# Kernel optimization log

Measured on AMD Instinct MI355X. Metric: run time of the kernel, lower is better.

Reference implementation:

```python
import jax, jax.numpy as jnp
import numpy as np

B, L, D, P = 4, 128, 256, 1024
TU, TB = 86400, 3600  # tu = 24*3600, time_bin = 3600
NEG = float(-2**32 + 1)


def setup_inputs() -> dict:
    key = jax.random.key(0)
    ks = jax.random.split(key, 16)
    src = jax.random.normal(ks[0], (B, L, D), jnp.float32)
    batch_seq_lens = jax.random.randint(ks[1], (B,), L // 2, L + 1, dtype=jnp.int32)
    ts = jnp.sort(jax.random.randint(ks[2], (B, L), 0, 864000, dtype=jnp.int32), axis=1)
    lts = ts + jax.random.randint(ks[3], (B, L), 0, 7200, dtype=jnp.int32)
    s = 0.02
    hour_emb = (jax.random.normal(ks[4], (TU // TB + 2, D), jnp.float32) * s).at[0].set(0.0)  # padding_idx=0
    day_emb = (jax.random.normal(ks[5], (8, D), jnp.float32) * s).at[0].set(0.0)              # padding_idx=0
    wq = jax.random.normal(ks[6], (D, D), jnp.float32) * s
    wk = jax.random.normal(ks[7], (D, D), jnp.float32) * s
    wv = jax.random.normal(ks[8], (D, D), jnp.float32) * s
    wf1 = jax.random.normal(ks[9], (D, D), jnp.float32) * s
    wf2 = jax.random.normal(ks[10], (D, D), jnp.float32) * s
    wdec = jax.random.uniform(ks[11], (P, D), jnp.float32, -0.1, 0.1)  # init_weights uniform(-0.1,0.1)
    z = jnp.zeros((D,), jnp.float32)
    return {
        'src': src, 'hour_emb': hour_emb, 'day_emb': day_emb,
        'wq': wq, 'bq': z, 'wk': wk, 'bk': z, 'wv': wv, 'bv': z,
        'g11': jnp.ones((D,), jnp.float32), 'b11': z,
        'wf1': wf1, 'bf1': z, 'wf2': wf2, 'bf2': z,
        'g12': jnp.ones((D,), jnp.float32), 'b12': z,
        'wdec': wdec, 'bdec': jnp.zeros((P,), jnp.float32),
        'batch_seq_lens': batch_seq_lens,
        'batch_input_seqs_ts': ts,
        'batch_label_seqs_ts': lts,
    }


def _ln(x, g, b):
    m = jnp.mean(x, axis=-1, keepdims=True)
    v = jnp.var(x, axis=-1, keepdims=True)
    return (x - m) * jax.lax.rsqrt(v + 1e-5) * g + b


def reference(src, hour_emb, day_emb, wq, bq, wk, bk, wv, bv, g11, b11,
              wf1, bf1, wf2, bf2, g12, b12, wdec, bdec,
              batch_seq_lens, batch_input_seqs_ts, batch_label_seqs_ts):
    ts, lts = batch_input_seqs_ts, batch_label_seqs_ts
    # per-pair time intervals, [B,L,L]
    diff = ts[:, :, None] - ts[:, None, :]
    hour = (diff % TU) // TB + 2
    # faithful to source: 'if i == j' compares batch index to row position
    hour = jnp.where((jnp.arange(B)[:, None] == jnp.arange(L)[None, :])[:, :, None], 1, hour)
    day = jnp.minimum(diff // TU + 1, 7)
    ldiff = lts[:, :, None] - ts[:, None, :]
    lhour = (ldiff % TU) // TB + 2
    lday = jnp.minimum(ldiff // TU + 1, 7)
    tril = jnp.tril(jnp.ones((L, L), bool))
    rows_valid = jnp.arange(L)[None, :] < batch_seq_lens[:, None]  # [B,L]
    valid = tril[None] & rows_valid[:, :, None]
    # index 0 == padding row (zero embedding), matching zeros-init + padding_idx=0
    hour = jnp.where(valid, hour, 0)
    day = jnp.where(valid, day, 0)
    lhour = jnp.where(valid, lhour, 0)
    lday = jnp.where(valid, lday, 0)
    hE = hour_emb[hour]    # [B,L,L,D]
    dE = day_emb[day]
    lhE = hour_emb[lhour]
    ldE = day_emb[lday]

    Q = src @ wq.T + bq
    K = src @ wk.T + bk
    V = src @ wv.T + bv
    aw = (jnp.einsum('bjd,bkd->bjk', Q, K)
          + jnp.einsum('bjkd,bjd->bjk', hE, Q)
          + jnp.einsum('bjkd,bjd->bjk', dE, Q)) / jnp.sqrt(jnp.float32(D))
    mask = (~tril)[None] | (~rows_valid)[:, :, None]
    aw = jnp.where(mask, NEG, aw)
    aw = jax.nn.softmax(aw, axis=-1)
    x = (jnp.einsum('bjk,bkd->bjd', aw, V)
         + jnp.einsum('bjk,bjkd->bjd', aw, hE)
         + jnp.einsum('bjk,bjkd->bjd', aw, dE))
    x = _ln(x + src, g11, b11)
    f = jnp.maximum(x @ wf1.T + bf1, 0.0) @ wf2.T + bf2  # dropout is identity at eval
    f = _ln(x + f, g12, b12)

    # out4[b,j,k,:] = f[b,k,:] + label interval embeddings
    out4 = f[:, None, :, :] + lhE + ldE            # [B,L,L,D]
    dec = out4 @ wdec.T + bdec                     # [B,L,L,P]
    counts = jnp.arange(1, L + 1, dtype=dec.dtype)
    pooled = jnp.einsum('bjkp,jk->bjp', dec, tril.astype(dec.dtype)) / counts[None, :, None]
    return pooled
```

## Files before the change

kernel.cpp:

```cpp
#include <hip/hip_runtime.h>
#include <hip/hip_bf16.h>

#define LL 128
#define DD 256
#define PP 1024
#define TU_C 86400
#define TB_C 3600
#define NEGF -4294967296.0f

#define FMA4(ACC_, SS_, WW_) { (ACC_).x += (SS_)*(WW_).x; (ACC_).y += (SS_)*(WW_).y; (ACC_).z += (SS_)*(WW_).z; (ACC_).w += (SS_)*(WW_).w; }
#define ADD4(ACC_, WW_) { (ACC_).x += (WW_).x; (ACC_).y += (WW_).y; (ACC_).z += (WW_).z; (ACC_).w += (WW_).w; }

__device__ __forceinline__ float wredSum(float v) {
#pragma unroll
  for (int o = 32; o; o >>= 1) v += __shfl_xor(v, o);
  return v;
}
__device__ __forceinline__ float wredMax(float v) {
#pragma unroll
  for (int o = 32; o; o >>= 1) v = fmaxf(v, __shfl_xor(v, o));
  return v;
}

__global__ __launch_bounds__(256) void k_wt(
    const float* __restrict__ wq, const float* __restrict__ wk,
    const float* __restrict__ wv, const float* __restrict__ wf1,
    const float* __restrict__ wf2, const float* __restrict__ wdec,
    float* __restrict__ wt)
{
  __shared__ float s[32][33];
  const int tile = blockIdx.x;
  const float* src; float* dst; int R, m;
  if (tile < 320) {
    const int mi = tile >> 6; m = tile & 63;
    src = (mi == 0) ? wq : (mi == 1) ? wk : (mi == 2) ? wv : (mi == 3) ? wf1 : wf2;
    dst = wt + mi * 65536; R = 256;
  } else {
    m = tile - 320; src = wdec; dst = wt + 327680; R = 1024;
  }
  const int sr = (m >> 3) * 32, sc0 = (m & 7) * 32;
  const int tx = threadIdx.x & 31, ty = threadIdx.x >> 5;
#pragma unroll
  for (int i = 0; i < 4; ++i)
    s[ty + 8 * i][tx] = src[(sr + ty + 8 * i) * 256 + sc0 + tx];
  __syncthreads();
#pragma unroll
  for (int i = 0; i < 4; ++i)
    dst[(sc0 + ty + 8 * i) * R + sr + tx] = s[tx][ty + 8 * i];
}

__global__ __launch_bounds__(256) void k_qkv(
    const float* __restrict__ src, const float* __restrict__ wt,
    const float* __restrict__ bq, const float* __restrict__ bk,
    const float* __restrict__ bv,
    float* __restrict__ Q, float* __restrict__ KT, float* __restrict__ V)
{
  __shared__ float xs[8][DD];
  __shared__ float ps[4][8][DD];
  const int t = threadIdx.x, l = t & 63, w = t >> 6;
  const int r0 = blockIdx.x * 8;
  const int mat = blockIdx.y;
  const float* wm = wt + mat * 65536;
  for (int i = t; i < 8 * DD; i += 256) xs[i >> 8][i & 255] = src[r0 * DD + i];
  __syncthreads();
  const int col = 4 * l;
  float4 acc[8];
#pragma unroll
  for (int r = 0; r < 8; ++r) acc[r] = (float4){0.f, 0.f, 0.f, 0.f};
  const int e0 = 64 * w;
  for (int e = e0; e < e0 + 64; e += 4) {
    float4 xr[8];
#pragma unroll
    for (int r = 0; r < 8; ++r) xr[r] = *(const float4*)&xs[r][e];
#pragma unroll
    for (int c = 0; c < 4; ++c) {
      const float4 w4 = *(const float4*)(wm + (e + c) * DD + col);
#pragma unroll
      for (int r = 0; r < 8; ++r) {
        const float xv = (c == 0) ? xr[r].x : (c == 1) ? xr[r].y : (c == 2) ? xr[r].z : xr[r].w;
        FMA4(acc[r], xv, w4)
      }
    }
  }
#pragma unroll
  for (int r = 0; r < 8; ++r) *(float4*)&ps[w][r][col] = acc[r];
  __syncthreads();
  const float* bi = (mat == 0) ? bq : (mat == 1) ? bk : bv;
#pragma unroll
  for (int g = 0; g < 2; ++g) {
    const int combo = g * 256 + t;
    const int r = combo >> 6, cgp = combo & 63;
    const int c4 = 4 * cgp;
    float4 o = *(const float4*)(bi + c4);
    ADD4(o, (*(const float4*)&ps[0][r][c4]))
    ADD4(o, (*(const float4*)&ps[1][r][c4]))
    ADD4(o, (*(const float4*)&ps[2][r][c4]))
    ADD4(o, (*(const float4*)&ps[3][r][c4]))
    const int rr = r0 + r;
    if (mat == 1) {
      const int bA = rr >> 7, kA = rr & 127;
      KT[bA * 32768 + (c4 + 0) * 128 + kA] = o.x;
      KT[bA * 32768 + (c4 + 1) * 128 + kA] = o.y;
      KT[bA * 32768 + (c4 + 2) * 128 + kA] = o.z;
      KT[bA * 32768 + (c4 + 3) * 128 + kA] = o.w;
    } else {
      float* op = (mat == 0) ? Q : V;
      *(float4*)(op + rr * DD + c4) = o;
    }
  }
}

__global__ __launch_bounds__(512) void k_attn(
    const float* __restrict__ Q, const float* __restrict__ KT,
    const float* __restrict__ Vm, const float* __restrict__ src,
    const float* __restrict__ hour_emb, const float* __restrict__ day_emb,
    const int* __restrict__ seq_lens, const int* __restrict__ ts_g,
    const float* __restrict__ g11, const float* __restrict__ b11,
    const float* __restrict__ wt1, const float* __restrict__ bf1,
    const float* __restrict__ wt2, const float* __restrict__ bf2,
    const float* __restrict__ g12, const float* __restrict__ b12,
    float* __restrict__ F)
{
  const int b = blockIdx.x >> 6;
  const int j0 = (blockIdx.x & 63) * 2;
  const int t = threadIdx.x, w = t >> 6, l = t & 63;
  const int col = 4 * l;
  __shared__ float qs[2][DD];
  __shared__ int   tsl[LL];
  __shared__ float qhd[2][34];
  __shared__ float whd[2][34];
  __shared__ float red[8];
  __shared__ float ss[2][LL];
  __shared__ float xs2[2][DD];
  __shared__ float hs2[2][DD];
  __shared__ float ps[8][2][DD];
  const int row0 = b * LL + j0;
  qs[t >> 8][t & 255] = Q[row0 * DD + t];
  if (t < LL) tsl[t] = ts_g[b * LL + t];
  if (t < 68) whd[t / 34][t % 34] = 0.f;
  __syncthreads();
  float kdot = 0.f;
  int krow = 0, kidx = 0;
  if (w < 4) {
    krow = w >> 1;
    kidx = ((w & 1) << 6) | l;
    const float* ktb = KT + b * 32768;
    float4 kd = {0.f,0.f,0.f,0.f};
#pragma unroll 8
    for (int e = 0; e < DD; e += 4) {
      const float4 q4 = *(const float4*)&qs[krow][e];
      const float* kp = ktb + e * LL + kidx;
      kd.x += q4.x * kp[0];
      kd.y += q4.y * kp[128];
      kd.z += q4.z * kp[256];
      kd.w += q4.w * kp[384];
    }
    kdot = (kd.x + kd.y) + (kd.z + kd.w);
  } else if (w < 6 && l < 34) {
    const int r = w - 4;
    const float* ep = (l < 26) ? (hour_emb + l * DD) : (day_emb + (l - 26) * DD);
    float4 ed = {0.f,0.f,0.f,0.f};
    for (int e = 0; e < DD; e += 4) {
      const float4 q4 = *(const float4*)&qs[r][e];
      const float4 e4 = *(const float4*)(ep + e);
      ed.x += q4.x * e4.x; ed.y += q4.y * e4.y;
      ed.z += q4.z * e4.z; ed.w += q4.w * e4.w;
    }
    qhd[r][l] = (ed.x + ed.y) + (ed.z + ed.w);
  }
  __syncthreads();
  const int len = seq_lens[b];
  float s = NEGF;
  int hidx = 0, didx = 0;
  if (w < 4) {
    const int jrow = j0 + krow;
    if (kidx <= jrow && jrow < len) {
      const int df = tsl[jrow] - tsl[kidx];
      hidx = (jrow == b) ? 1 : ((df % TU_C) / TB_C + 2);
      didx = min(df / TU_C + 1, 7);
      s = (kdot + qhd[krow][hidx] + qhd[krow][26 + didx]) * 0.0625f;
    }
    const float mv = wredMax(s);
    if (l == 0) red[w] = mv;
  }
  __syncthreads();
  float p = 0.f;
  if (w < 4) {
    const float m = fmaxf(red[2 * krow], red[2 * krow + 1]);
    p = expf(s - m);
    const float sv = wredSum(p);
    if (l == 0) red[4 + w] = sv;
  }
  __syncthreads();
  if (w < 4) {
    const float Z = red[4 + 2 * krow] + red[5 + 2 * krow];
    const float aw = p / Z;
    ss[krow][kidx] = aw;
    atomicAdd(&whd[krow][hidx], aw);
    atomicAdd(&whd[krow][26 + didx], aw);
  }
  __syncthreads();
  {
    float4 a0 = {0.f,0.f,0.f,0.f}, a1 = {0.f,0.f,0.f,0.f};
    const float* vb = Vm + b * LL * DD + col;
    const int k0 = 16 * w;
#pragma unroll
    for (int kk = 0; kk < 16; ++kk) {
      const int k = k0 + kk;
      const float4 v4 = *(const float4*)(vb + k * DD);
      FMA4(a0, ss[0][k], v4)
      FMA4(a1, ss[1][k], v4)
    }
    if (w == 0) {
#pragma unroll
      for (int i = 0; i < 26; ++i)
        FMA4(a0, whd[0][i], *(const float4*)(hour_emb + i * DD + col))
    } else if (w == 1) {
#pragma unroll
      for (int i = 0; i < 26; ++i)
        FMA4(a1, whd[1][i], *(const float4*)(hour_emb + i * DD + col))
    } else if (w == 2) {
#pragma unroll
      for (int i = 0; i < 8; ++i)
        FMA4(a0, whd[0][26 + i], *(const float4*)(day_emb + i * DD + col))
      const float4 s4 = *(const float4*)(src + row0 * DD + col);
      ADD4(a0, s4)
    } else if (w == 3) {
#pragma unroll
      for (int i = 0; i < 8; ++i)
        FMA4(a1, whd[1][26 + i], *(const float4*)(day_emb + i * DD + col))
      const float4 s4 = *(const float4*)(src + (row0 + 1) * DD + col);
      ADD4(a1, s4)
    }
    *(float4*)&ps[w][0][col] = a0;
    *(float4*)&ps[w][1][col] = a1;
  }
  __syncthreads();
  if (w < 2) {
    float4 x = *(const float4*)&ps[0][w][col];
#pragma unroll
    for (int i = 1; i < 8; ++i) ADD4(x, (*(const float4*)&ps[i][w][col]))
    const float sm = wredSum(x.x + x.y + x.z + x.w);
    const float sq = wredSum(x.x*x.x + x.y*x.y + x.z*x.z + x.w*x.w);
    const float mean = sm * (1.f / DD);
    const float rstd = rsqrtf(sq * (1.f / DD) - mean * mean + 1e-5f);
    const float4 g4 = *(const float4*)(g11 + col);
    const float4 b4 = *(const float4*)(b11 + col);
    x.x = (x.x - mean) * rstd * g4.x + b4.x;
    x.y = (x.y - mean) * rstd * g4.y + b4.y;
    x.z = (x.z - mean) * rstd * g4.z + b4.z;
    x.w = (x.w - mean) * rstd * g4.w + b4.w;
    *(float4*)&xs2[w][col] = x;
  }
  __syncthreads();
  {
    float4 a0 = {0.f,0.f,0.f,0.f}, a1 = {0.f,0.f,0.f,0.f};
    const int e0 = 32 * w;
#pragma unroll 8
    for (int ee = 0; ee < 32; ++ee) {
      const int e = e0 + ee;
      const float4 w4 = *(const float4*)(wt1 + e * DD + col);
      FMA4(a0, xs2[0][e], w4)
      FMA4(a1, xs2[1][e], w4)
    }
    *(float4*)&ps[w][0][col] = a0;
    *(float4*)&ps[w][1][col] = a1;
  }
  __syncthreads();
  if (w < 2) {
    float4 h = *(const float4*)(bf1 + col);
#pragma unroll
    for (int i = 0; i < 8; ++i) ADD4(h, (*(const float4*)&ps[i][w][col]))
    h.x = fmaxf(h.x, 0.f); h.y = fmaxf(h.y, 0.f);
    h.z = fmaxf(h.z, 0.f); h.w = fmaxf(h.w, 0.f);
    *(float4*)&hs2[w][col] = h;
  }
  __syncthreads();
  {
    float4 a0 = {0.f,0.f,0.f,0.f}, a1 = {0.f,0.f,0.f,0.f};
    const int e0 = 32 * w;
#pragma unroll 8
    for (int ee = 0; ee < 32; ++ee) {
      const int e = e0 + ee;
      const float4 w4 = *(const float4*)(wt2 + e * DD + col);
      FMA4(a0, hs2[0][e], w4)
      FMA4(a1, hs2[1][e], w4)
    }
    *(float4*)&ps[w][0][col] = a0;
    *(float4*)&ps[w][1][col] = a1;
  }
  __syncthreads();
  if (w < 2) {
    float4 o = *(const float4*)(bf2 + col);
#pragma unroll
    for (int i = 0; i < 8; ++i) ADD4(o, (*(const float4*)&ps[i][w][col]))
    const float4 xr = *(const float4*)&xs2[w][col];
    ADD4(o, xr)
    const float sm = wredSum(o.x + o.y + o.z + o.w);
    const float sq = wredSum(o.x*o.x + o.y*o.y + o.z*o.z + o.w*o.w);
    const float mean = sm * (1.f / DD);
    const float rstd = rsqrtf(sq * (1.f / DD) - mean * mean + 1e-5f);
    const float4 g4 = *(const float4*)(g12 + col);
    const float4 b4 = *(const float4*)(b12 + col);
    o.x = (o.x - mean) * rstd * g4.x + b4.x;
    o.y = (o.y - mean) * rstd * g4.y + b4.y;
    o.z = (o.z - mean) * rstd * g4.z + b4.z;
    o.w = (o.w - mean) * rstd * g4.w + b4.w;
    *(float4*)(F + (row0 + w) * DD + col) = o;
  }
}

__global__ __launch_bounds__(256) void k_decf(
    const float* __restrict__ F,
    const float* __restrict__ hour_emb, const float* __restrict__ day_emb,
    const int* __restrict__ seq_lens, const int* __restrict__ ts_g,
    const int* __restrict__ lts_g,
    const float* __restrict__ wtd, const float* __restrict__ bdec,
    float* __restrict__ out)
{
  const int c0 = blockIdx.x * 256;
  const int r0g = blockIdx.y * 8;
  const int b = r0g >> 7, j0 = r0g & 127;
  const int t = threadIdx.x, l = t & 63, w = t >> 6;
  __shared__ float xs[8][DD];
  __shared__ float cnt[8][34];
  __shared__ float ps[4][8][DD];
  for (int i = t; i < 8 * 34; i += 256) (&cnt[0][0])[i] = 0.f;
  __syncthreads();
  const int len = seq_lens[b];
  const int* ts = ts_g + b * LL;
  const int* lts = lts_g + b * LL;
#pragma unroll
  for (int p = 0; p < 4; ++p) {
    const int idx = p * 256 + t;
    const int jj = idx >> 7, k = idx & 127, j = j0 + jj;
    if (k <= j && j < len) {
      const int ld = lts[j] - ts[k];
      atomicAdd(&cnt[jj][(ld % TU_C) / TB_C + 2], 1.f);
      atomicAdd(&cnt[jj][26 + min(ld / TU_C + 1, 7)], 1.f);
    }
  }
  __syncthreads();
  {
    float he[26], de[8];
#pragma unroll
    for (int i = 0; i < 26; ++i) he[i] = hour_emb[i * DD + t];
#pragma unroll
    for (int i = 0; i < 8; ++i)  de[i] = day_emb[i * DD + t];
    const float* fb = F + b * LL * DD + t;
    float A0 = 0.f, A1 = 0.f, A2 = 0.f, A3 = 0.f;
#pragma unroll 4
    for (int k = 0; k < j0; k += 4) {
      A0 += fb[(k + 0) * DD]; A1 += fb[(k + 1) * DD];
      A2 += fb[(k + 2) * DD]; A3 += fb[(k + 3) * DD];
    }
    float gacc = (A0 + A1) + (A2 + A3);
#pragma unroll
    for (int jj = 0; jj < 8; ++jj) {
      gacc += fb[(j0 + jj) * DD];
      float s0 = 0.f, s1 = 0.f;
#pragma unroll
      for (int i = 0; i < 26; i += 2) {
        s0 += cnt[jj][i] * he[i]; s1 += cnt[jj][i + 1] * he[i + 1];
      }
#pragma unroll
      for (int i = 0; i < 8; i += 2) {
        s0 += cnt[jj][26 + i] * de[i]; s1 += cnt[jj][27 + i] * de[i + 1];
      }
      xs[jj][t] = (gacc + s0 + s1) / (float)(j0 + jj + 1);
    }
  }
  __syncthreads();
  const int col = c0 + 4 * l;
  float4 acc[8];
#pragma unroll
  for (int r = 0; r < 8; ++r) acc[r] = (float4){0.f, 0.f, 0.f, 0.f};
  const int e0 = 64 * w;
  for (int e = e0; e < e0 + 64; e += 4) {
    float4 xr[8];
#pragma unroll
    for (int r = 0; r < 8; ++r) xr[r] = *(const float4*)&xs[r][e];
#pragma unroll
    for (int c = 0; c < 4; ++c) {
      const float4 w4 = *(const float4*)(wtd + (e + c) * PP + col);
#pragma unroll
      for (int r = 0; r < 8; ++r) {
        const float xv = (c == 0) ? xr[r].x : (c == 1) ? xr[r].y : (c == 2) ? xr[r].z : xr[r].w;
        FMA4(acc[r], xv, w4)
      }
    }
  }
#pragma unroll
  for (int r = 0; r < 8; ++r) *(float4*)&ps[w][r][4 * l] = acc[r];
  __syncthreads();
#pragma unroll
  for (int g = 0; g < 2; ++g) {
    const int combo = g * 256 + t;
    const int r = combo >> 6, cgp = combo & 63;
    const int c4 = 4 * cgp;
    float4 o = *(const float4*)(bdec + c0 + c4);
    ADD4(o, (*(const float4*)&ps[0][r][c4]))
    ADD4(o, (*(const float4*)&ps[1][r][c4]))
    ADD4(o, (*(const float4*)&ps[2][r][c4]))
    ADD4(o, (*(const float4*)&ps[3][r][c4]))
    *(float4*)(out + (r0g + r) * PP + c0 + c4) = o;
  }
}

extern "C" void kernel_launch(void* const* d_in, const int* in_sizes, int n_in,
                              void* d_out, int out_size, void* d_ws, size_t ws_size,
                              hipStream_t stream)
{
  (void)in_sizes; (void)n_in; (void)out_size; (void)ws_size;
  const float* src      = (const float*)d_in[0];
  const float* hour_emb = (const float*)d_in[1];
  const float* day_emb  = (const float*)d_in[2];
  const float* wq  = (const float*)d_in[3];
  const float* bq  = (const float*)d_in[4];
  const float* wk  = (const float*)d_in[5];
  const float* bk  = (const float*)d_in[6];
  const float* wv  = (const float*)d_in[7];
  const float* bv  = (const float*)d_in[8];
  const float* g11 = (const float*)d_in[9];
  const float* b11 = (const float*)d_in[10];
  const float* wf1 = (const float*)d_in[11];
  const float* bf1 = (const float*)d_in[12];
  const float* wf2 = (const float*)d_in[13];
  const float* bf2 = (const float*)d_in[14];
  const float* g12 = (const float*)d_in[15];
  const float* b12 = (const float*)d_in[16];
  const float* wdec = (const float*)d_in[17];
  const float* bdec = (const float*)d_in[18];
  const int* seq_lens = (const int*)d_in[19];
  const int* ts  = (const int*)d_in[20];
  const int* lts = (const int*)d_in[21];
  float* out = (float*)d_out;
  float* ws = (float*)d_ws;
  float* WT = ws;
  float* Q  = ws + 589824;
  float* KT = ws + 720896;
  float* V  = ws + 851968;
  float* F  = ws + 983040;

  k_wt  <<<576, 256, 0, stream>>>(wq, wk, wv, wf1, wf2, wdec, WT);
  k_qkv <<<dim3(64, 3), 256, 0, stream>>>(src, WT, bq, bk, bv, Q, KT, V);
  k_attn<<<256, 512, 0, stream>>>(Q, KT, V, src, hour_emb, day_emb, seq_lens, ts,
                                  g11, b11, WT + 196608, bf1, WT + 262144, bf2,
                                  g12, b12, F);
  k_decf<<<dim3(4, 64), 256, 0, stream>>>(F, hour_emb, day_emb, seq_lens, ts, lts,
                                          WT + 327680, bdec, out);
}
```

Baseline: 50.36 us.

## Fuse weight transpose and QKV projection into one kernel launch

Merges the weight-transpose kernel and the QKV projection kernel into a single launch. Blocks 0-191 compute Q/K/V by reading the untransposed wq/wk/wv directly, staging 16-column chunks into LDS, while the remaining blocks transpose only wf1, wf2 and wdec for later kernels. This drops one kernel launch and the dependency of QKV on a transposed copy of its own weights. In exchange the QKV GEMM loop synchronises 16 times per block and does strided, poorly coalesced global loads of the weights.

```diff
diff --git a/kernel.cpp b/kernel.cpp
--- a/kernel.cpp
+++ b/kernel.cpp
@@ -22,91 +22,81 @@
   return v;
 }
 
-__global__ __launch_bounds__(256) void k_wt(
+__global__ __launch_bounds__(256) void k_qkv2(
     const float* __restrict__ wq, const float* __restrict__ wk,
     const float* __restrict__ wv, const float* __restrict__ wf1,
     const float* __restrict__ wf2, const float* __restrict__ wdec,
-    float* __restrict__ wt)
-{
-  __shared__ float s[32][33];
-  const int tile = blockIdx.x;
-  const float* src; float* dst; int R, m;
-  if (tile < 320) {
-    const int mi = tile >> 6; m = tile & 63;
-    src = (mi == 0) ? wq : (mi == 1) ? wk : (mi == 2) ? wv : (mi == 3) ? wf1 : wf2;
-    dst = wt + mi * 65536; R = 256;
-  } else {
-    m = tile - 320; src = wdec; dst = wt + 327680; R = 1024;
-  }
-  const int sr = (m >> 3) * 32, sc0 = (m & 7) * 32;
-  const int tx = threadIdx.x & 31, ty = threadIdx.x >> 5;
-#pragma unroll
-  for (int i = 0; i < 4; ++i)
-    s[ty + 8 * i][tx] = src[(sr + ty + 8 * i) * 256 + sc0 + tx];
-  __syncthreads();
-#pragma unroll
-  for (int i = 0; i < 4; ++i)
-    dst[(sc0 + ty + 8 * i) * R + sr + tx] = s[tx][ty + 8 * i];
-}
-
-__global__ __launch_bounds__(256) void k_qkv(
-    const float* __restrict__ src, const float* __restrict__ wt,
+    const float* __restrict__ src,
     const float* __restrict__ bq, const float* __restrict__ bk,
     const float* __restrict__ bv,
+    float* __restrict__ WT,
     float* __restrict__ Q, float* __restrict__ KT, float* __restrict__ V)
 {
+  const int bx = blockIdx.x;
+  const int t = threadIdx.x;
+  if (bx >= 192) {
+    __shared__ float s[32][33];
+    const int tile = bx - 192;
+    const float* sw; float* dst; int R, m;
+    if (tile < 64)       { sw = wf1;  dst = WT + 196608; R = 256;  m = tile; }
+    else if (tile < 128) { sw = wf2;  dst = WT + 262144; R = 256;  m = tile - 64; }
+    else                 { sw = wdec; dst = WT + 327680; R = 1024; m = tile - 128; }
+    const int sr = (m >> 3) * 32, sc0 = (m & 7) * 32;
+    const int tx = t & 31, ty = t >> 5;
+#pragma unroll
+    for (int i = 0; i < 4; ++i)
+      s[ty + 8 * i][tx] = sw[(sr + ty + 8 * i) * 256 + sc0 + tx];
+    __syncthreads();
+#pragma unroll
+    for (int i = 0; i < 4; ++i)
+      dst[(sc0 + ty + 8 * i) * R + sr + tx] = s[tx][ty + 8 * i];
+    return;
+  }
+  const int mat = bx >> 6;
+  const int r0 = (bx & 63) * 8;
+  const float* wm = (mat == 0) ? wq : (mat == 1) ? wk : wv;
   __shared__ float xs[8][DD];
-  __shared__ float ps[4][8][DD];
-  const int t = threadIdx.x, l = t & 63, w = t >> 6;
-  const int r0 = blockIdx.x * 8;
-  const int mat = blockIdx.y;
-  const float* wm = wt + mat * 65536;
+  __shared__ float wlds[16][260];
   for (int i = t; i < 8 * DD; i += 256) xs[i >> 8][i & 255] = src[r0 * DD + i];
-  __syncthreads();
-  const int col = 4 * l;
-  float4 acc[8];
-#pragma unroll
-  for (int r = 0; r < 8; ++r) acc[r] = (float4){0.f, 0.f, 0.f, 0.f};
-  const int e0 = 64 * w;
-  for (int e = e0; e < e0 + 64; e += 4) {
-    float4 xr[8];
-#pragma unroll
-    for (int r = 0; r < 8; ++r) xr[r] = *(const float4*)&xs[r][e];
-#pragma unroll
-    for (int c = 0; c < 4; ++c) {
-      const float4 w4 = *(const float4*)(wm + (e + c) * DD + col);
-#pragma unroll
-      for (int r = 0; r < 8; ++r) {
-        const float xv = (c == 0) ? xr[r].x : (c == 1) ? xr[r].y : (c == 2) ? xr[r].z : xr[r].w;
-        FMA4(acc[r], xv, w4)
-      }
-    }
-  }
-#pragma unroll
-  for (int r = 0; r < 8; ++r) *(float4*)&ps[w][r][col] = acc[r];
-  __syncthreads();
+  const int cg = t & 63, w = t >> 6;
+  const int col4 = 4 * cg;
+  const int rA = 2 * w, rB = rA + 1;
+  float4 a0 = {0.f,0.f,0.f,0.f}, a1 = {0.f,0.f,0.f,0.f};
+  for (int c = 0; c < 16; ++c) {
+    const int e1 = c * 16;
+    __syncthreads();
+#pragma unroll
+    for (int it = 0; it < 16; ++it) {
+      const int idx = it * 256 + t;
+      const int ccol = idx >> 4, eo = idx & 15;
+      wlds[eo][ccol] = wm[ccol * 256 + e1 + eo];
+    }
+    __syncthreads();
+#pragma unroll
+    for (int eo = 0; eo < 16; ++eo) {
+      const float4 w4 = *(const float4*)&wlds[eo][col4];
+      FMA4(a0, xs[rA][e1 + eo], w4)
+      FMA4(a1, xs[rB][e1 + eo], w4)
+    }
+  }
   const float* bi = (mat == 0) ? bq : (mat == 1) ? bk : bv;
-#pragma unroll
-  for (int g = 0; g < 2; ++g) {
-    const int combo = g * 256 + t;
-    const int r = combo >> 6, cgp = combo & 63;
-    const int c4 = 4 * cgp;
-    float4 o = *(const float4*)(bi + c4);
-    ADD4(o, (*(const float4*)&ps[0][r][c4]))
-    ADD4(o, (*(const float4*)&ps[1][r][c4]))
-    ADD4(o, (*(const float4*)&ps[2][r][c4]))
-    ADD4(o, (*(const float4*)&ps[3][r][c4]))
-    const int rr = r0 + r;
-    if (mat == 1) {
-      const int bA = rr >> 7, kA = rr & 127;
-      KT[bA * 32768 + (c4 + 0) * 128 + kA] = o.x;
-      KT[bA * 32768 + (c4 + 1) * 128 + kA] = o.y;
-      KT[bA * 32768 + (c4 + 2) * 128 + kA] = o.z;
-      KT[bA * 32768 + (c4 + 3) * 128 + kA] = o.w;
-    } else {
-      float* op = (mat == 0) ? Q : V;
-      *(float4*)(op + rr * DD + c4) = o;
-    }
+  const float4 b4v = *(const float4*)(bi + col4);
+  ADD4(a0, b4v) ADD4(a1, b4v)
+  const int gA = r0 + rA, gB = r0 + rB;
+  if (mat == 1) {
+    const int bA = gA >> 7, kA = gA & 127;
+    KT[bA * 32768 + (col4 + 0) * 128 + kA] = a0.x;
+    KT[bA * 32768 + (col4 + 1) * 128 + kA] = a0.y;
+    KT[bA * 32768 + (col4 + 2) * 128 + kA] = a0.z;
+    KT[bA * 32768 + (col4 + 3) * 128 + kA] = a0.w;
+    KT[bA * 32768 + (col4 + 0) * 128 + kA + 1] = a1.x;
+    KT[bA * 32768 + (col4 + 1) * 128 + kA + 1] = a1.y;
+    KT[bA * 32768 + (col4 + 2) * 128 + kA + 1] = a1.z;
+    KT[bA * 32768 + (col4 + 3) * 128 + kA + 1] = a1.w;
+  } else {
+    float* o = (mat == 0) ? Q : V;
+    *(float4*)(o + gA * DD + col4) = a0;
+    *(float4*)(o + gB * DD + col4) = a1;
   }
 }
 
@@ -442,8 +432,8 @@
   float* V  = ws + 851968;
   float* F  = ws + 983040;
 
-  k_wt  <<<576, 256, 0, stream>>>(wq, wk, wv, wf1, wf2, wdec, WT);
-  k_qkv <<<dim3(64, 3), 256, 0, stream>>>(src, WT, bq, bk, bv, Q, KT, V);
+  k_qkv2<<<576, 256, 0, stream>>>(wq, wk, wv, wf1, wf2, wdec, src,
+                                  bq, bk, bv, WT, Q, KT, V);
   k_attn<<<256, 512, 0, stream>>>(Q, KT, V, src, hour_emb, day_emb, seq_lens, ts,
                                   g11, b11, WT + 196608, bf1, WT + 262144, bf2,
                                   g12, b12, F);
```

New measurement: 50.84 us. No clear change (+0.9%).
